# Optimization experiments

Hardware: AMD Instinct MI355X
Metric: run time of the kernel (lower is better)

The kernel has to match this reference:

```python
import jax, jax.numpy as jnp
import numpy as np
from jax import lax

MAXW = 4  # spans cover j in [i, min(i+4, max_len)) -> widths 1..4


def setup_inputs() -> dict:
    key = jax.random.key(0)
    ks = jax.random.split(key, 8)
    B, L, H = 64, 512, 256
    Hd = H // 2  # dynamicLSTM hidden = kernel_num/2
    s = 0.05
    feats = jax.random.normal(ks[0], (B, L, H), dtype=jnp.float32)
    lens = jax.random.randint(ks[1], (B,), 1, L + 1)
    W_ih = jax.random.normal(ks[2], (4 * Hd, H), dtype=jnp.float32) * s
    W_hh = jax.random.normal(ks[3], (4 * Hd, Hd), dtype=jnp.float32) * s
    b_ih = jax.random.normal(ks[4], (4 * Hd,), dtype=jnp.float32) * s
    b_hh = jax.random.normal(ks[5], (4 * Hd,), dtype=jnp.float32) * s
    W_tri = jax.random.normal(ks[6], (2, Hd), dtype=jnp.float32) * s
    b_tri = jax.random.normal(ks[7], (2,), dtype=jnp.float32) * s
    return {"feats": feats, "W_ih": W_ih, "W_hh": W_hh, "b_ih": b_ih,
            "b_hh": b_hh, "W_tri": W_tri, "b_tri": b_tri, "lens": lens}


def _build_tag_graph(feats, W_ih, W_hh, b_ih, b_hh, W_tri, b_tri, lens):
    B, Lmax, H = feats.shape
    Hd = W_hh.shape[1]
    starts = jnp.arange(Lmax)
    idx = starts[:, None] + jnp.arange(MAXW)[None, :]              # (L, 4)
    in_range = idx < Lmax
    win = feats[:, jnp.minimum(idx, Lmax - 1)] * in_range[None, :, :, None]  # (B, L, 4, H)
    x = win.transpose(2, 0, 1, 3).reshape(MAXW, B * Lmax, H)       # steps-major

    def step(carry, xt):
        h, c = carry
        gates = xt @ W_ih.T + b_ih + h @ W_hh.T + b_hh
        i_, f_, g_, o_ = jnp.split(gates, 4, axis=-1)  # torch gate order i,f,g,o
        c = jax.nn.sigmoid(f_) * c + jax.nn.sigmoid(i_) * jnp.tanh(g_)
        h = jax.nn.sigmoid(o_) * jnp.tanh(c)
        return (h, c), h

    h0 = jnp.zeros((B * Lmax, Hd), feats.dtype)
    _, hs = lax.scan(step, (h0, h0), x)                            # (4, B*L, Hd)
    hs = hs.reshape(MAXW, B, Lmax, Hd).transpose(1, 2, 0, 3)       # (B, L, 4, Hd); [...,t,:] = hidden after t+1 steps

    # effective packed length per span: total = clip(lens - i, 0, w); pack uses max(total, 1)
    w = jnp.arange(1, MAXW + 1)                                    # span widths
    rem = lens[:, None] - starts[None, :]                          # (B, L)
    total = jnp.clip(rem[:, :, None], 0, w[None, None, :])         # (B, L, 4)
    Lsel = jnp.maximum(total, 1)
    row_mask = (total > 0).astype(feats.dtype)
    h_span = jnp.take_along_axis(hs, (Lsel - 1)[..., None], axis=2)  # (B, L, 4, Hd)

    emit = (h_span @ W_tri.T + b_tri) * row_mask[..., None]        # (B, L, 4, 2)
    # scatter emit[b, i, w-1] into span_scores[b, i, i+w-1]; drop spans past max_len
    valid_span = in_range  # j = i + (w-1) < Lmax
    emit = emit * valid_span[None, :, :, None]
    j_clamped = jnp.minimum(idx, Lmax - 1)
    span_scores = jnp.zeros((B, Lmax, Lmax, 2), feats.dtype)
    span_scores = span_scores.at[:, starts[:, None], j_clamped].add(emit)
    return span_scores


def reference(feats, W_ih, W_hh, b_ih, b_hh, W_tri, b_tri, lens):
    return _build_tag_graph(feats, W_ih, W_hh, b_ih, b_hh, W_tri, b_tri, lens)
```

## Files before the change

kernel.cpp:

```cpp
#include <hip/hip_runtime.h>
#include <cstddef>

#define NB 64
#define LL 512
#define HH 256
#define HD 128
#define NG 512
#define TI 16

typedef _Float16 half_t;
typedef _Float16 half8 __attribute__((ext_vector_type(8)));
typedef _Float16 half4 __attribute__((ext_vector_type(4)));
typedef float f32x4 __attribute__((ext_vector_type(4)));

#define MFMA16(a, b, c) __builtin_amdgcn_mfma_f32_16x16x32_f16((a), (b), (c), 0, 0, 0)

#define FP 264
#define XP 522
#define HFP 132
#define HBP 136

__device__ __forceinline__ float sigm(float x)  { return 1.0f / (1.0f + __expf(-x)); }
__device__ __forceinline__ float tanhf_(float x){ return 2.0f / (1.0f + __expf(-2.0f * x)) - 1.0f; }

__global__ void prep_weights(const float* __restrict__ Wih, const float* __restrict__ Whh,
                             const float* __restrict__ bih, const float* __restrict__ bhh,
                             half_t* __restrict__ WihH, half_t* __restrict__ WhhH,
                             float* __restrict__ bsum)
{
    const int idx = blockIdx.x * 256 + threadIdx.x;
    if (idx < NG * HH) WihH[idx] = (half_t)Wih[idx];
    if (idx < NG * HD) WhhH[idx] = (half_t)Whh[idx];
    if (idx < NG)      bsum[idx] = bih[idx] + bhh[idx];
}

__global__ __launch_bounds__(256, 2) void span_lstm_mfma(
    const float* __restrict__ feats, const half_t* __restrict__ WihH,
    const half_t* __restrict__ WhhH, const float* __restrict__ bsum,
    const float* __restrict__ W_tri, const float* __restrict__ b_tri,
    const int* __restrict__ lens, float* __restrict__ out)
{
    __shared__ __align__(16) half_t sFeatb[32 * FP];
    __shared__ __align__(16) float  sXG[20 * XP];
    __shared__ __align__(16) float  sHf[16 * HFP];
    __shared__ __align__(16) half_t sHb[16 * HBP];
    __shared__ float sEmit[2][32];

    const int tid = threadIdx.x;
    const int b  = blockIdx.x >> 5;
    const int i0 = (blockIdx.x & 31) * TI;
    const int lens_b = lens[b];

    for (int idx = tid; idx < 20 * 64; idx += 256) {
        const int p  = idx >> 6;
        const int k4 = (idx & 63) << 2;
        const int gp = i0 + p;
        float4 v = make_float4(0.f, 0.f, 0.f, 0.f);
        if (gp < LL) v = *(const float4*)(feats + ((size_t)b * LL + gp) * HH + k4);
        half4 hv = {(half_t)v.x, (half_t)v.y, (half_t)v.z, (half_t)v.w};
        *(half4*)(&sFeatb[p * FP + k4]) = hv;
    }
    __syncthreads();

    const int lane = tid & 63, wv = tid >> 6;
    const int lm = lane & 15;
    const int lq = lane >> 4;

    {
        half8 afr[2][8];
        #pragma unroll
        for (int mt = 0; mt < 2; ++mt)
            #pragma unroll
            for (int kf = 0; kf < 8; ++kf)
                afr[mt][kf] = *(const half8*)(&sFeatb[(16 * mt + lm) * FP + kf * 32 + lq * 8]);

        const int gwv = wv * 128;
        for (int nt = 0; nt < 8; ++nt) {
            const int gb = gwv + nt * 16;
            const float bs = bsum[gb + lm];
            f32x4 acc0 = {0.f, 0.f, 0.f, 0.f}, acc1 = {0.f, 0.f, 0.f, 0.f};
            #pragma unroll
            for (int kf = 0; kf < 8; ++kf) {
                const half8 bfr = *(const half8*)(WihH + (size_t)(gb + lm) * HH + kf * 32 + lq * 8);
                acc0 = MFMA16(afr[0][kf], bfr, acc0);
                acc1 = MFMA16(afr[1][kf], bfr, acc1);
            }
            #pragma unroll
            for (int r = 0; r < 4; ++r)
                sXG[(lq * 4 + r) * XP + gb + lm] = acc0[r] + bs;
            if (lq == 0) {
                #pragma unroll
                for (int r = 0; r < 4; ++r)
                    sXG[(16 + r) * XP + gb + lm] = acc1[r] + bs;
            }
        }
    }

    const int j0 = 32 * wv;
    half8 bf2[2][4][4];
    #pragma unroll
    for (int jt = 0; jt < 2; ++jt)
        #pragma unroll
        for (int ta = 0; ta < 4; ++ta)
            #pragma unroll
            for (int kf = 0; kf < 4; ++kf)
                bf2[jt][ta][kf] = *(const half8*)(WhhH + (size_t)(ta * HD + j0 + jt * 16 + lm) * HD
                                                  + kf * 32 + lq * 8);
    __syncthreads();

    float cc[2][4] = {{0.f, 0.f, 0.f, 0.f}, {0.f, 0.f, 0.f, 0.f}};

    for (int t = 0; t < 4; ++t) {
        float accg[2][4][4];
        if (t > 0) {
            half8 ah[4];
            #pragma unroll
            for (int kf = 0; kf < 4; ++kf)
                ah[kf] = *(const half8*)(&sHb[lm * HBP + kf * 32 + lq * 8]);
            #pragma unroll
            for (int jt = 0; jt < 2; ++jt)
                #pragma unroll
                for (int ta = 0; ta < 4; ++ta) {
                    f32x4 a = {0.f, 0.f, 0.f, 0.f};
                    #pragma unroll
                    for (int kf = 0; kf < 4; ++kf)
                        a = MFMA16(ah[kf], bf2[jt][ta][kf], a);
                    #pragma unroll
                    for (int r = 0; r < 4; ++r) accg[jt][ta][r] = a[r];
                }
        } else {
            #pragma unroll
            for (int jt = 0; jt < 2; ++jt)
                #pragma unroll
                for (int ta = 0; ta < 4; ++ta)
                    #pragma unroll
                    for (int r = 0; r < 4; ++r) accg[jt][ta][r] = 0.f;
        }
        #pragma unroll
        for (int jt = 0; jt < 2; ++jt)
            #pragma unroll
            for (int ta = 0; ta < 4; ++ta)
                #pragma unroll
                for (int r = 0; r < 4; ++r)
                    accg[jt][ta][r] += sXG[(lq * 4 + r + t) * XP + ta * HD + j0 + jt * 16 + lm];

        float hh[2][4];
        #pragma unroll
        for (int jt = 0; jt < 2; ++jt)
            #pragma unroll
            for (int r = 0; r < 4; ++r) {
                const float ig = sigm(accg[jt][0][r]);
                const float fg = sigm(accg[jt][1][r]);
                const float gg = tanhf_(accg[jt][2][r]);
                const float og = sigm(accg[jt][3][r]);
                cc[jt][r] = fg * cc[jt][r] + ig * gg;
                hh[jt][r] = og * tanhf_(cc[jt][r]);
            }
        __syncthreads();
        #pragma unroll
        for (int jt = 0; jt < 2; ++jt)
            #pragma unroll
            for (int r = 0; r < 4; ++r) {
                const int s = lq * 4 + r, j = j0 + jt * 16 + lm;
                sHf[s * HFP + j] = hh[jt][r];
                sHb[s * HBP + j] = (half_t)hh[jt][r];
            }
        __syncthreads();

        if (tid < 128) {
            const int es = tid & 15, etag = (tid >> 4) & 1, ekc = tid >> 5;
            float part = 0.f;
            #pragma unroll
            for (int jj = 0; jj < 8; ++jj) {
                const float4 hv = *(const float4*)(&sHf[es * HFP + ekc * 32 + 4 * jj]);
                const float4 wt = *(const float4*)(W_tri + (size_t)etag * HD + ekc * 32 + 4 * jj);
                part += hv.x * wt.x + hv.y * wt.y + hv.z * wt.z + hv.w * wt.w;
            }
            part += __shfl_down(part, 32);
            if ((tid & 32) == 0) sEmit[tid >> 6][tid & 31] = part;
        }
        __syncthreads();
        if (tid < 32) {
            const int es = tid & 15, etag = tid >> 4;
            const int i = i0 + es;
            const int rem = lens_b - i;
            const int sc = t + 1;
            if (rem > 0 && sc <= rem) {
                const float e = sEmit[0][tid] + sEmit[1][tid] + b_tri[etag];
                const int mm  = rem < 4 ? rem : 4;
                const int whi = (sc >= mm) ? 4 : sc;
                for (int w2 = sc; w2 <= whi; ++w2) {
                    const int jj2 = i + w2 - 1;
                    if (jj2 < LL)
                        out[(((size_t)b * LL + i) * LL + jj2) * 2 + etag] = e;
                }
            }
        }
    }
}

extern "C" void kernel_launch(void* const* d_in, const int* in_sizes, int n_in,
                              void* d_out, int out_size, void* d_ws, size_t ws_size,
                              hipStream_t stream)
{
    const float* feats = (const float*)d_in[0];
    const float* W_ih  = (const float*)d_in[1];
    const float* W_hh  = (const float*)d_in[2];
    const float* b_ih  = (const float*)d_in[3];
    const float* b_hh  = (const float*)d_in[4];
    const float* W_tri = (const float*)d_in[5];
    const float* b_tri = (const float*)d_in[6];
    const int*   lens  = (const int*)d_in[7];
    float* out = (float*)d_out;

    hipMemsetAsync(out, 0, (size_t)out_size * sizeof(float), stream);

    half_t* WihH = (half_t*)d_ws;
    half_t* WhhH = WihH + (size_t)NG * HH;
    float*  bsum = (float*)(WhhH + (size_t)NG * HD);

    prep_weights<<<(NG * HH + 255) / 256, 256, 0, stream>>>(W_ih, W_hh, b_ih, b_hh,
                                                            WihH, WhhH, bsum);
    span_lstm_mfma<<<NB * (LL / TI), 256, 0, stream>>>(feats, WihH, WhhH, bsum,
                                                       W_tri, b_tri, lens, out);
}
```

Baseline: 291.7 us.

## Fuse output zeroing into LSTM kernel, widen blocks, shuffle-reduce emit

Drops the separate hipMemsetAsync and has each block zero its own 16-row slab of the output with vector stores, spread across the four timesteps. Block size doubles to 512 threads so each wave owns 16 hidden units. sFeatb now aliases sXG, and sHb is double-buffered to cut per-step barriers from three to one. The tri-projection is done with in-register shuffle reductions into a small partials array, and all span writes are deferred to the end of the kernel. The main risk is ordering: the zero stores and the later scattered score writes from the same block must not conflict, and higher register use per thread may limit occupancy.

```diff
diff --git a/kernel.cpp b/kernel.cpp
--- a/kernel.cpp
+++ b/kernel.cpp
@@ -17,7 +17,6 @@
 
 #define FP 264
 #define XP 522
-#define HFP 132
 #define HBP 136
 
 __device__ __forceinline__ float sigm(float x)  { return 1.0f / (1.0f + __expf(-x)); }
@@ -34,24 +33,29 @@
     if (idx < NG)      bsum[idx] = bih[idx] + bhh[idx];
 }
 
-__global__ __launch_bounds__(256, 2) void span_lstm_mfma(
+__global__ __launch_bounds__(512, 4) void span_lstm_mfma(
     const float* __restrict__ feats, const half_t* __restrict__ WihH,
     const half_t* __restrict__ WhhH, const float* __restrict__ bsum,
     const float* __restrict__ W_tri, const float* __restrict__ b_tri,
     const int* __restrict__ lens, float* __restrict__ out)
 {
-    __shared__ __align__(16) half_t sFeatb[32 * FP];
     __shared__ __align__(16) float  sXG[20 * XP];
-    __shared__ __align__(16) float  sHf[16 * HFP];
-    __shared__ __align__(16) half_t sHb[16 * HBP];
-    __shared__ float sEmit[2][32];
+    __shared__ __align__(16) half_t sHb[2][16 * HBP];
+    __shared__ __align__(16) float  sEmitP[4][2][TI][8];
+
+    half_t* sFeatb = (half_t*)sXG;
 
     const int tid = threadIdx.x;
     const int b  = blockIdx.x >> 5;
     const int i0 = (blockIdx.x & 31) * TI;
     const int lens_b = lens[b];
 
-    for (int idx = tid; idx < 20 * 64; idx += 256) {
+    const int lane = tid & 63, wv = tid >> 6;
+    const int lm = lane & 15;
+    const int lq = lane >> 4;
+    const int jw = wv * 16;
+
+    for (int idx = tid; idx < 20 * 64; idx += 512) {
         const int p  = idx >> 6;
         const int k4 = (idx & 63) << 2;
         const int gp = i0 + p;
@@ -62,138 +66,134 @@
     }
     __syncthreads();
 
-    const int lane = tid & 63, wv = tid >> 6;
-    const int lm = lane & 15;
-    const int lq = lane >> 4;
-
-    {
-        half8 afr[2][8];
-        #pragma unroll
-        for (int mt = 0; mt < 2; ++mt)
-            #pragma unroll
-            for (int kf = 0; kf < 8; ++kf)
-                afr[mt][kf] = *(const half8*)(&sFeatb[(16 * mt + lm) * FP + kf * 32 + lq * 8]);
-
-        const int gwv = wv * 128;
-        for (int nt = 0; nt < 8; ++nt) {
-            const int gb = gwv + nt * 16;
-            const float bs = bsum[gb + lm];
-            f32x4 acc0 = {0.f, 0.f, 0.f, 0.f}, acc1 = {0.f, 0.f, 0.f, 0.f};
-            #pragma unroll
-            for (int kf = 0; kf < 8; ++kf) {
-                const half8 bfr = *(const half8*)(WihH + (size_t)(gb + lm) * HH + kf * 32 + lq * 8);
-                acc0 = MFMA16(afr[0][kf], bfr, acc0);
-                acc1 = MFMA16(afr[1][kf], bfr, acc1);
-            }
+    half8 afr[2][8];
+    #pragma unroll
+    for (int mt = 0; mt < 2; ++mt)
+        #pragma unroll
+        for (int kf = 0; kf < 8; ++kf)
+            afr[mt][kf] = *(const half8*)(&sFeatb[(16 * mt + lm) * FP + kf * 32 + lq * 8]);
+    __syncthreads();
+
+    #pragma unroll
+    for (int ta = 0; ta < 4; ++ta) {
+        const int gb = ta * HD + jw;
+        const float bs = bsum[gb + lm];
+        f32x4 acc0 = {0.f, 0.f, 0.f, 0.f}, acc1 = {0.f, 0.f, 0.f, 0.f};
+        #pragma unroll
+        for (int kf = 0; kf < 8; ++kf) {
+            const half8 bfr = *(const half8*)(WihH + (size_t)(gb + lm) * HH + kf * 32 + lq * 8);
+            acc0 = MFMA16(afr[0][kf], bfr, acc0);
+            acc1 = MFMA16(afr[1][kf], bfr, acc1);
+        }
+        #pragma unroll
+        for (int r = 0; r < 4; ++r)
+            sXG[(lq * 4 + r) * XP + gb + lm] = acc0[r] + bs;
+        if (lq == 0) {
             #pragma unroll
             for (int r = 0; r < 4; ++r)
-                sXG[(lq * 4 + r) * XP + gb + lm] = acc0[r] + bs;
-            if (lq == 0) {
-                #pragma unroll
-                for (int r = 0; r < 4; ++r)
-                    sXG[(16 + r) * XP + gb + lm] = acc1[r] + bs;
-            }
-        }
-    }
-
-    const int j0 = 32 * wv;
-    half8 bf2[2][4][4];
-    #pragma unroll
-    for (int jt = 0; jt < 2; ++jt)
-        #pragma unroll
-        for (int ta = 0; ta < 4; ++ta)
-            #pragma unroll
-            for (int kf = 0; kf < 4; ++kf)
-                bf2[jt][ta][kf] = *(const half8*)(WhhH + (size_t)(ta * HD + j0 + jt * 16 + lm) * HD
-                                                  + kf * 32 + lq * 8);
-    __syncthreads();
-
-    float cc[2][4] = {{0.f, 0.f, 0.f, 0.f}, {0.f, 0.f, 0.f, 0.f}};
-
+                sXG[(16 + r) * XP + gb + lm] = acc1[r] + bs;
+        }
+    }
+
+    half8 bf2[4][4];
+    #pragma unroll
+    for (int ta = 0; ta < 4; ++ta)
+        #pragma unroll
+        for (int kf = 0; kf < 4; ++kf)
+            bf2[ta][kf] = *(const half8*)(WhhH + (size_t)(ta * HD + jw + lm) * HD
+                                          + kf * 32 + lq * 8);
+
+    const float wt0 = W_tri[jw + lm];
+    const float wt1 = W_tri[HD + jw + lm];
+
+    f32x4* ob4 = (f32x4*)(out + ((size_t)b * LL + i0) * (LL * 2));
+    const f32x4 zz = {0.f, 0.f, 0.f, 0.f};
+
+    float cc4[4] = {0.f, 0.f, 0.f, 0.f};
+
+    #pragma unroll
     for (int t = 0; t < 4; ++t) {
-        float accg[2][4][4];
+        float accg[4][4];
         if (t > 0) {
             half8 ah[4];
             #pragma unroll
             for (int kf = 0; kf < 4; ++kf)
-                ah[kf] = *(const half8*)(&sHb[lm * HBP + kf * 32 + lq * 8]);
-            #pragma unroll
-            for (int jt = 0; jt < 2; ++jt)
+                ah[kf] = *(const half8*)(&sHb[(t - 1) & 1][lm * HBP + kf * 32 + lq * 8]);
+            #pragma unroll
+            for (int ta = 0; ta < 4; ++ta) {
+                f32x4 a = {0.f, 0.f, 0.f, 0.f};
                 #pragma unroll
-                for (int ta = 0; ta < 4; ++ta) {
-                    f32x4 a = {0.f, 0.f, 0.f, 0.f};
-                    #pragma unroll
-                    for (int kf = 0; kf < 4; ++kf)
-                        a = MFMA16(ah[kf], bf2[jt][ta][kf], a);
-                    #pragma unroll
-                    for (int r = 0; r < 4; ++r) accg[jt][ta][r] = a[r];
-                }
+                for (int kf = 0; kf < 4; ++kf)
+                    a = MFMA16(ah[kf], bf2[ta][kf], a);
+                #pragma unroll
+                for (int r = 0; r < 4; ++r) accg[ta][r] = a[r];
+            }
         } else {
-            #pragma unroll
-            for (int jt = 0; jt < 2; ++jt)
-                #pragma unroll
-                for (int ta = 0; ta < 4; ++ta)
-                    #pragma unroll
-                    for (int r = 0; r < 4; ++r) accg[jt][ta][r] = 0.f;
-        }
-        #pragma unroll
-        for (int jt = 0; jt < 2; ++jt)
             #pragma unroll
             for (int ta = 0; ta < 4; ++ta)
                 #pragma unroll
-                for (int r = 0; r < 4; ++r)
-                    accg[jt][ta][r] += sXG[(lq * 4 + r + t) * XP + ta * HD + j0 + jt * 16 + lm];
-
-        float hh[2][4];
-        #pragma unroll
-        for (int jt = 0; jt < 2; ++jt)
-            #pragma unroll
-            for (int r = 0; r < 4; ++r) {
-                const float ig = sigm(accg[jt][0][r]);
-                const float fg = sigm(accg[jt][1][r]);
-                const float gg = tanhf_(accg[jt][2][r]);
-                const float og = sigm(accg[jt][3][r]);
-                cc[jt][r] = fg * cc[jt][r] + ig * gg;
-                hh[jt][r] = og * tanhf_(cc[jt][r]);
+                for (int r = 0; r < 4; ++r) accg[ta][r] = 0.f;
+        }
+        #pragma unroll
+        for (int ta = 0; ta < 4; ++ta)
+            #pragma unroll
+            for (int r = 0; r < 4; ++r)
+                accg[ta][r] += sXG[(lq * 4 + r + t) * XP + ta * HD + jw + lm];
+
+        float hh[4];
+        #pragma unroll
+        for (int r = 0; r < 4; ++r) {
+            const float ig = sigm(accg[0][r]);
+            const float fg = sigm(accg[1][r]);
+            const float gg = tanhf_(accg[2][r]);
+            const float og = sigm(accg[3][r]);
+            cc4[r] = fg * cc4[r] + ig * gg;
+            hh[r]  = og * tanhf_(cc4[r]);
+        }
+
+        if (t < 3) {
+            #pragma unroll
+            for (int r = 0; r < 4; ++r)
+                sHb[t & 1][(lq * 4 + r) * HBP + jw + lm] = (half_t)hh[r];
+        }
+
+        #pragma unroll
+        for (int r = 0; r < 4; ++r) {
+            float e0 = hh[r] * wt0;
+            float e1 = hh[r] * wt1;
+            e0 += __shfl_xor(e0, 1);  e1 += __shfl_xor(e1, 1);
+            e0 += __shfl_xor(e0, 2);  e1 += __shfl_xor(e1, 2);
+            e0 += __shfl_xor(e0, 4);  e1 += __shfl_xor(e1, 4);
+            e0 += __shfl_xor(e0, 8);  e1 += __shfl_xor(e1, 8);
+            if (lm == 0) {
+                sEmitP[t][0][lq * 4 + r][wv] = e0;
+                sEmitP[t][1][lq * 4 + r][wv] = e1;
             }
+        }
+
+        ob4[(t << 10) + tid]       = zz;
+        ob4[(t << 10) + 512 + tid] = zz;
+
         __syncthreads();
-        #pragma unroll
-        for (int jt = 0; jt < 2; ++jt)
-            #pragma unroll
-            for (int r = 0; r < 4; ++r) {
-                const int s = lq * 4 + r, j = j0 + jt * 16 + lm;
-                sHf[s * HFP + j] = hh[jt][r];
-                sHb[s * HBP + j] = (half_t)hh[jt][r];
-            }
-        __syncthreads();
-
-        if (tid < 128) {
-            const int es = tid & 15, etag = (tid >> 4) & 1, ekc = tid >> 5;
-            float part = 0.f;
-            #pragma unroll
-            for (int jj = 0; jj < 8; ++jj) {
-                const float4 hv = *(const float4*)(&sHf[es * HFP + ekc * 32 + 4 * jj]);
-                const float4 wt = *(const float4*)(W_tri + (size_t)etag * HD + ekc * 32 + 4 * jj);
-                part += hv.x * wt.x + hv.y * wt.y + hv.z * wt.z + hv.w * wt.w;
-            }
-            part += __shfl_down(part, 32);
-            if ((tid & 32) == 0) sEmit[tid >> 6][tid & 31] = part;
-        }
-        __syncthreads();
-        if (tid < 32) {
-            const int es = tid & 15, etag = tid >> 4;
-            const int i = i0 + es;
-            const int rem = lens_b - i;
-            const int sc = t + 1;
-            if (rem > 0 && sc <= rem) {
-                const float e = sEmit[0][tid] + sEmit[1][tid] + b_tri[etag];
-                const int mm  = rem < 4 ? rem : 4;
-                const int whi = (sc >= mm) ? 4 : sc;
-                for (int w2 = sc; w2 <= whi; ++w2) {
-                    const int jj2 = i + w2 - 1;
-                    if (jj2 < LL)
-                        out[(((size_t)b * LL + i) * LL + jj2) * 2 + etag] = e;
-                }
+    }
+
+    if (tid < 128) {
+        const int es = tid & 15, etag = (tid >> 4) & 1, t = tid >> 5;
+        const float* pp = sEmitP[t][etag][es];
+        float e = b_tri[etag];
+        #pragma unroll
+        for (int w8 = 0; w8 < 8; ++w8) e += pp[w8];
+
+        const int i = i0 + es;
+        const int rem = lens_b - i;
+        const int sc = t + 1;
+        if (rem > 0 && sc <= rem) {
+            const int mm  = rem < 4 ? rem : 4;
+            const int whi = (sc >= mm) ? 4 : sc;
+            for (int w2 = sc; w2 <= whi; ++w2) {
+                const int jj2 = i + w2 - 1;
+                if (jj2 < LL)
+                    out[(((size_t)b * LL + i) * LL + jj2) * 2 + etag] = e;
             }
         }
     }
@@ -213,7 +213,6 @@
     const int*   lens  = (const int*)d_in[7];
     float* out = (float*)d_out;
 
-    hipMemsetAsync(out, 0, (size_t)out_size * sizeof(float), stream);
 
     half_t* WihH = (half_t*)d_ws;
     half_t* WhhH = WihH + (size_t)NG * HH;
@@ -221,6 +220,6 @@
 
     prep_weights<<<(NG * HH + 255) / 256, 256, 0, stream>>>(W_ih, W_hh, b_ih, b_hh,
                                                             WihH, WhhH, bsum);
-    span_lstm_mfma<<<NB * (LL / TI), 256, 0, stream>>>(feats, WihH, WhhH, bsum,
+    span_lstm_mfma<<<NB * (LL / TI), 512, 0, stream>>>(feats, WihH, WhhH, bsum,
                                                        W_tri, b_tri, lens, out);
 }
```

Result: faster. 260.3 us (-10.8%).
